# Performance work log

Measured on AMD Instinct MI355X. Metric: run time of the kernel, lower is better.

The kernel has to match this reference:

```python
import jax, jax.numpy as jnp
import numpy as np
from jax import lax


def squash(x, axis=-1):
    sq = jnp.sum(x * x, axis=axis, keepdims=True)
    n = jnp.sqrt(sq)
    return jnp.tanh(n) * x / (n + 1e-8)


def setup_inputs() -> dict:
    key = jax.random.key(0)
    ks = jax.random.split(key, 12)
    B = 2048
    x = jax.random.normal(ks[0], (B, 64, 22, 22), dtype=jnp.float32)
    conv1_w = 0.02 * jax.random.normal(ks[1], (256, 64, 9, 9), dtype=jnp.float32)
    conv1_b = jnp.zeros((256,), jnp.float32)
    pc_w = 0.02 * jax.random.normal(ks[2], (48, 256, 8, 8), dtype=jnp.float32)  # out_channels*num_conv_units=8*6
    pc_b = jnp.zeros((48,), jnp.float32)
    W_digit = 0.01 * jax.random.normal(ks[3], (1, 2, 96, 16, 8), dtype=jnp.float32)  # (1,out_caps,in_caps,out_dim,in_dim)
    dec_w1 = 0.05 * jax.random.normal(ks[4], (512, 32), dtype=jnp.float32)  # in = out_dim*num_classes = 16*2
    dec_b1 = jnp.zeros((512,), jnp.float32)
    dec_w2 = 0.03 * jax.random.normal(ks[5], (1024, 512), dtype=jnp.float32)
    dec_b2 = jnp.zeros((1024,), jnp.float32)
    dec_w3 = 0.03 * jax.random.normal(ks[6], (256, 1024), dtype=jnp.float32)  # fusion_dim=256
    dec_b3 = jnp.zeros((256,), jnp.float32)
    return dict(x=x, conv1_w=conv1_w, conv1_b=conv1_b, pc_w=pc_w, pc_b=pc_b,
                W_digit=W_digit, dec_w1=dec_w1, dec_b1=dec_b1, dec_w2=dec_w2,
                dec_b2=dec_b2, dec_w3=dec_w3, dec_b3=dec_b3)


def reference(x, conv1_w, conv1_b, pc_w, pc_b, W_digit,
              dec_w1, dec_b1, dec_w2, dec_b2, dec_w3, dec_b3):
    DN = ('NCHW', 'OIHW', 'NCHW')
    NUM_ROUTING = 2
    OUT_CAPS = 2
    # conv1 + relu: (B,64,22,22) -> (B,256,14,14)
    out = lax.conv_general_dilated(x, conv1_w, (1, 1), 'VALID', dimension_numbers=DN)
    out = jax.nn.relu(out + conv1_b[None, :, None, None])
    # primary caps conv: -> (B,48,4,4)
    pc = lax.conv_general_dilated(out, pc_w, (2, 2), 'VALID', dimension_numbers=DN)
    pc = pc + pc_b[None, :, None, None]
    B = pc.shape[0]
    u = squash(pc.reshape(B, -1, 8), axis=-1)  # (B, 96, 8)
    # u_hat: W (out_caps,in_caps,out_dim,in_dim) x u (B,in_caps,in_dim) -> (B,out_caps,in_caps,out_dim)
    u_hat = jnp.einsum('oidk,bik->boid', W_digit[0], u)
    tmp = lax.stop_gradient(u_hat)
    b = jnp.zeros((B, OUT_CAPS, 96, 1), u_hat.dtype)
    for _ in range(NUM_ROUTING - 1):
        c = jax.nn.softmax(b, axis=1)                     # over out_caps
        v = squash(jnp.sum(c * tmp, axis=2))              # (B,out_caps,out_dim)
        b = jnp.einsum('boid,bod->boi', tmp, v)[..., None]
    c = jax.nn.softmax(b, axis=1)
    v = squash(jnp.sum(c * u_hat, axis=2))                # (B,out_caps,out_dim)
    logits = jnp.linalg.norm(v, axis=-1)                  # (B,out_caps)
    pred = jax.nn.one_hot(jnp.argmax(logits, axis=1), OUT_CAPS, dtype=v.dtype)  # (B,out_caps)
    h = (v * pred[:, :, None]).reshape(B, -1)             # (B, out_caps*out_dim)
    h = jax.nn.relu(h @ dec_w1.T + dec_b1)
    h = jax.nn.relu(h @ dec_w2.T + dec_b2)
    recon = jax.nn.sigmoid(h @ dec_w3.T + dec_b3)
    return logits, recon
```

## Files before the change

### kernel.cpp

```cpp
#include <hip/hip_runtime.h>
#include <cstdint>
#include <cstddef>

typedef short short8 __attribute__((ext_vector_type(8)));
typedef short short4v __attribute__((ext_vector_type(4)));
typedef float f32x16 __attribute__((ext_vector_type(16)));
typedef float f32x4 __attribute__((ext_vector_type(4)));

__device__ inline unsigned short bf16_rne(float x) {
    unsigned u = __float_as_uint(x);
    unsigned r = u + 0x7FFFu + ((u >> 16) & 1u);
    return (unsigned short)(r >> 16);
}
__device__ inline float bf16_to_f(unsigned short h) {
    return __uint_as_float(((unsigned)h) << 16);
}

__global__ void reorder_wf_kernel(const float* __restrict__ w, unsigned short* __restrict__ wf) {
    int idx = blockIdx.x * 256 + threadIdx.x;
    if (idx >= 324 * 8 * 64 * 8) return;
    int j   = idx & 7;
    int l   = (idx >> 3) & 63;
    int nc  = (idx >> 9) & 7;
    int ksg = idx >> 12;
    int cc  = ksg / 81;
    int tap = ksg - cc * 81;
    int ci  = cc * 16 + ((l >> 5) << 3) + j;
    int co  = nc * 32 + (l & 31);
    float v = w[(co * 64 + ci) * 81 + tap];
    unsigned short hi = bf16_rne(v);
    unsigned short lo = bf16_rne(v - bf16_to_f(hi));
    size_t base = ((size_t)(ksg * 8 + nc)) * 1024;
    wf[base + l * 8 + j]       = hi;
    wf[base + 512 + l * 8 + j] = lo;
}

__global__ void reorder_pcwf_kernel(const float* __restrict__ w, unsigned short* __restrict__ wf) {
    int idx = blockIdx.x * 256 + threadIdx.x;
    if (idx >= 1572864) return;
    int j     = idx & 7;
    int l     = (idx >> 3) & 63;
    int plane = (idx >> 9) & 1;
    int rest  = idx >> 10;
    int ct    = rest % 3;
    int rest2 = rest / 3;
    int tap   = rest2 & 63;
    int cc    = rest2 >> 6;
    int co = ct * 16 + (l & 15);
    int ci = cc * 32 + ((l >> 4) << 3) + j;
    float v = w[((size_t)co * 256 + ci) * 64 + tap];
    unsigned short hi = bf16_rne(v);
    unsigned short out = plane ? bf16_rne(v - bf16_to_f(hi)) : hi;
    wf[idx] = out;
}

#define RS 36

__global__ __launch_bounds__(256, 2) void conv1_mfma_kernel(
    const float* __restrict__ x, const unsigned short* __restrict__ wf,
    const float* __restrict__ b1, float* __restrict__ c1o, int c0)
{
    __shared__ unsigned short Xs[484 * RS];
    const int t  = threadIdx.x;
    const int l  = t & 63;
    const int w  = t >> 6;
    const int il = blockIdx.x >> 1;
    const int nb = blockIdx.x & 1;
    const int bg = c0 + il;
    const int ncol = nb * 4 + w;
    const int lane31 = l & 31;
    const int kg = l >> 5;
    const int co = ncol * 32 + lane31;
    const float bias = b1[co];

    int am[7];
#pragma unroll
    for (int mt = 0; mt < 7; ++mt) {
        int p  = mt * 32 + lane31;
        int pp = (p < 196) ? p : 0;
        int oh = pp / 14, ow = pp - oh * 14;
        am[mt] = (oh * 22 + ow) * RS + kg * 8;
    }
    const char* wfb = (const char*)wf;
    const int boff = ncol * 2048 + l * 16;

    f32x16 acc[7];
#pragma unroll
    for (int mt = 0; mt < 7; ++mt) acc[mt] = (f32x16)(0.f);

    for (int cc = 0; cc < 4; ++cc) {
        __syncthreads();
        for (int i = t; i < 16 * 121; i += 256) {
            int ci = i / 121;
            int sq = i - ci * 121;
            const float4 v = *(const float4*)(x + ((size_t)bg * 64 + cc * 16 + ci) * 484 + sq * 4);
#pragma unroll
            for (int e = 0; e < 4; ++e) {
                float xv = ((const float*)&v)[e];
                unsigned short hi = bf16_rne(xv);
                unsigned short lo = bf16_rne(xv - bf16_to_f(hi));
                int s = sq * 4 + e;
                Xs[s * RS + ci]      = hi;
                Xs[s * RS + 16 + ci] = lo;
            }
        }
        __syncthreads();

        const int ksgb = cc * 81;
        short8 bh0 = *(const short8*)(wfb + (size_t)ksgb * 16384 + boff);
        short8 bl0 = *(const short8*)(wfb + (size_t)ksgb * 16384 + 1024 + boff);

        for (int tap = 0; tap < 81; ++tap) {
            int kn = ksgb + tap + 1; if (kn > 323) kn = 323;
            short8 bh1 = *(const short8*)(wfb + (size_t)kn * 16384 + boff);
            short8 bl1 = *(const short8*)(wfb + (size_t)kn * 16384 + 1024 + boff);

            const int kh = tap / 9, kw = tap - kh * 9;
            const int toff = (kh * 22 + kw) * RS;
#pragma unroll
            for (int mt = 0; mt < 7; ++mt) {
                const int a = am[mt] + toff;
                short4v h0 = *(const short4v*)(Xs + a);
                short4v h1 = *(const short4v*)(Xs + a + 4);
                short4v q0 = *(const short4v*)(Xs + a + 16);
                short4v q1 = *(const short4v*)(Xs + a + 20);
                short8 Ah = __builtin_shufflevector(h0, h1, 0, 1, 2, 3, 4, 5, 6, 7);
                short8 Al = __builtin_shufflevector(q0, q1, 0, 1, 2, 3, 4, 5, 6, 7);
                acc[mt] = __builtin_amdgcn_mfma_f32_32x32x16_bf16(Ah, bh0, acc[mt], 0, 0, 0);
                acc[mt] = __builtin_amdgcn_mfma_f32_32x32x16_bf16(Ah, bl0, acc[mt], 0, 0, 0);
                acc[mt] = __builtin_amdgcn_mfma_f32_32x32x16_bf16(Al, bh0, acc[mt], 0, 0, 0);
                acc[mt] = __builtin_amdgcn_mfma_f32_32x32x16_bf16(Al, bl0, acc[mt], 0, 0, 0);
            }
            bh0 = bh1; bl0 = bl1;
        }
    }

#pragma unroll
    for (int mt = 0; mt < 7; ++mt) {
#pragma unroll
        for (int r = 0; r < 16; ++r) {
            int p = mt * 32 + (r & 3) + ((r >> 2) << 3) + kg * 4;
            if (p < 196) {
                float v = acc[mt][r] + bias;
                c1o[((size_t)il * 196 + p) * 256 + co] = fmaxf(v, 0.f);
            }
        }
    }
}

#define PC_RS 36

__global__ __launch_bounds__(256, 2) void pc_mfma_kernel(
    const float* __restrict__ c1o, const unsigned short* __restrict__ pcwf,
    const float* __restrict__ pcb, float* __restrict__ pco)
{
    __shared__ unsigned short Xh[196 * PC_RS];
    __shared__ unsigned short Xl[196 * PC_RS];
    const int t  = threadIdx.x;
    const int l  = t & 63;
    const int w  = t >> 6;
    const int il = blockIdx.x;
    const int pos = l & 15;
    const int kg  = l >> 4;
    const int oh = pos >> 2, ow = pos & 3;
    const char* wb = (const char*)pcwf;

    f32x4 acc0 = (f32x4)(0.f), acc1 = (f32x4)(0.f), acc2 = (f32x4)(0.f);

    for (int cc = 0; cc < 8; ++cc) {
        __syncthreads();
        for (int q = t; q < 1568; q += 256) {
            int p  = q >> 3;
            int c4 = (q & 7) << 2;
            const float4 v = *(const float4*)(c1o + ((size_t)il * 196 + p) * 256 + cc * 32 + c4);
            short4v hv, lv;
#pragma unroll
            for (int e = 0; e < 4; ++e) {
                float xv = ((const float*)&v)[e];
                unsigned short hi = bf16_rne(xv);
                hv[e] = (short)hi;
                lv[e] = (short)bf16_rne(xv - bf16_to_f(hi));
            }
            *(short4v*)(Xh + p * PC_RS + c4) = hv;
            *(short4v*)(Xl + p * PC_RS + c4) = lv;
        }
        __syncthreads();

        short8 Bh0[3], Bl0[3], Bh1[3], Bl1[3];
        {
            const char* bp = wb + ((size_t)(cc * 64 + w) * 6) * 1024 + l * 16;
#pragma unroll
            for (int ct = 0; ct < 3; ++ct) {
                Bh0[ct] = *(const short8*)(bp + ct * 2048);
                Bl0[ct] = *(const short8*)(bp + ct * 2048 + 1024);
            }
        }
        for (int tt = 0; tt < 16; ++tt) {
            const int tap = tt * 4 + w;
            const int tapn = (tt == 15) ? tap : (tap + 4);
            const char* bpn = wb + ((size_t)(cc * 64 + tapn) * 6) * 1024 + l * 16;
#pragma unroll
            for (int ct = 0; ct < 3; ++ct) {
                Bh1[ct] = *(const short8*)(bpn + ct * 2048);
                Bl1[ct] = *(const short8*)(bpn + ct * 2048 + 1024);
            }
            const int kh = tap >> 3, kw = tap & 7;
            const int pix = (2 * oh + kh) * 14 + (2 * ow + kw);
            const int a = pix * PC_RS + kg * 8;
            short4v h0 = *(const short4v*)(Xh + a);
            short4v h1 = *(const short4v*)(Xh + a + 4);
            short4v q0 = *(const short4v*)(Xl + a);
            short4v q1 = *(const short4v*)(Xl + a + 4);
            short8 Ah = __builtin_shufflevector(h0, h1, 0, 1, 2, 3, 4, 5, 6, 7);
            short8 Al = __builtin_shufflevector(q0, q1, 0, 1, 2, 3, 4, 5, 6, 7);

            acc0 = __builtin_amdgcn_mfma_f32_16x16x32_bf16(Ah, Bh0[0], acc0, 0, 0, 0);
            acc0 = __builtin_amdgcn_mfma_f32_16x16x32_bf16(Ah, Bl0[0], acc0, 0, 0, 0);
            acc0 = __builtin_amdgcn_mfma_f32_16x16x32_bf16(Al, Bh0[0], acc0, 0, 0, 0);
            acc0 = __builtin_amdgcn_mfma_f32_16x16x32_bf16(Al, Bl0[0], acc0, 0, 0, 0);
            acc1 = __builtin_amdgcn_mfma_f32_16x16x32_bf16(Ah, Bh0[1], acc1, 0, 0, 0);
            acc1 = __builtin_amdgcn_mfma_f32_16x16x32_bf16(Ah, Bl0[1], acc1, 0, 0, 0);
            acc1 = __builtin_amdgcn_mfma_f32_16x16x32_bf16(Al, Bh0[1], acc1, 0, 0, 0);
            acc1 = __builtin_amdgcn_mfma_f32_16x16x32_bf16(Al, Bl0[1], acc1, 0, 0, 0);
            acc2 = __builtin_amdgcn_mfma_f32_16x16x32_bf16(Ah, Bh0[2], acc2, 0, 0, 0);
            acc2 = __builtin_amdgcn_mfma_f32_16x16x32_bf16(Ah, Bl0[2], acc2, 0, 0, 0);
            acc2 = __builtin_amdgcn_mfma_f32_16x16x32_bf16(Al, Bh0[2], acc2, 0, 0, 0);
            acc2 = __builtin_amdgcn_mfma_f32_16x16x32_bf16(Al, Bl0[2], acc2, 0, 0, 0);
#pragma unroll
            for (int ct = 0; ct < 3; ++ct) { Bh0[ct] = Bh1[ct]; Bl0[ct] = Bl1[ct]; }
        }
    }

    __syncthreads();
    float* R = (float*)Xh;
#pragma unroll
    for (int ct = 0; ct < 3; ++ct) {
        f32x4 a = (ct == 0) ? acc0 : (ct == 1) ? acc1 : acc2;
#pragma unroll
        for (int r = 0; r < 4; ++r)
            R[(((w * 3 + ct) * 64) + l) * 4 + r] = a[r];
    }
    __syncthreads();
    for (int idx = t; idx < 768; idx += 256) {
        int pp = idx & 15, co = idx >> 4;
        int ct = co >> 4, col = co & 15;
        int lane = ((pp >> 2) << 4) | col, reg = pp & 3;
        float s = 0.f;
#pragma unroll
        for (int w4 = 0; w4 < 4; ++w4)
            s += R[(((w4 * 3 + ct) * 64) + lane) * 4 + reg];
        pco[(size_t)il * 768 + idx] = s + pcb[co];
    }
}

__global__ __launch_bounds__(64) void caps_kernel(
    const float* __restrict__ pco, const float* __restrict__ Wd,
    float* __restrict__ logits_out, float* __restrict__ hbuf, int c0) {
    __shared__ float u_s[96][8];
    __shared__ float uh[2][96][16];
    __shared__ float vv[2][16];
    __shared__ float cc2[2][96];
    __shared__ float lg_s[2];
    const int t = threadIdx.x;
    const int il = blockIdx.x;

    for (int cap = t; cap < 96; cap += 64) {
        float xr[8];
        float n2 = 0.f;
#pragma unroll
        for (int k = 0; k < 8; ++k) {
            xr[k] = pco[(size_t)il * 768 + cap * 8 + k];
            n2 = fmaf(xr[k], xr[k], n2);
        }
        float nr = sqrtf(n2);
        float sc = tanhf(nr) / (nr + 1e-8f);
#pragma unroll
        for (int k = 0; k < 8; ++k) u_s[cap][k] = xr[k] * sc;
    }
    __syncthreads();
    for (int j = t; j < 3072; j += 64) {
        int d = j & 15;
        int oi = j >> 4;
        int i = oi % 96;
        int o = oi / 96;
        float acc = 0.f;
#pragma unroll
        for (int k = 0; k < 8; ++k)
            acc = fmaf(Wd[(size_t)j * 8 + k], u_s[i][k], acc);
        uh[o][i][d] = acc;
    }
    __syncthreads();
    const int o = t >> 4, d = t & 15;
    if (t < 32) {
        float s = 0.f;
        for (int i = 0; i < 96; ++i) s += 0.5f * uh[o][i][d];
        float n2 = s * s;
        n2 += __shfl_xor(n2, 1); n2 += __shfl_xor(n2, 2);
        n2 += __shfl_xor(n2, 4); n2 += __shfl_xor(n2, 8);
        float nr = sqrtf(n2);
        vv[o][d] = tanhf(nr) * s / (nr + 1e-8f);
    }
    __syncthreads();
    for (int j = t; j < 192; j += 64) {
        int oo = j / 96, ii = j - oo * 96;
        float bsum = 0.f;
#pragma unroll
        for (int dd = 0; dd < 16; ++dd)
            bsum = fmaf(uh[oo][ii][dd], vv[oo][dd], bsum);
        cc2[oo][ii] = bsum;
    }
    __syncthreads();
    for (int ii = t; ii < 96; ii += 64) {
        float b0 = cc2[0][ii], b1v = cc2[1][ii];
        float m = fmaxf(b0, b1v);
        float e0 = expf(b0 - m), e1 = expf(b1v - m);
        float inv = 1.f / (e0 + e1);
        cc2[0][ii] = e0 * inv;
        cc2[1][ii] = e1 * inv;
    }
    __syncthreads();
    if (t < 32) {
        float s = 0.f;
        for (int i = 0; i < 96; ++i) s = fmaf(cc2[o][i], uh[o][i][d], s);
        float n2 = s * s;
        n2 += __shfl_xor(n2, 1); n2 += __shfl_xor(n2, 2);
        n2 += __shfl_xor(n2, 4); n2 += __shfl_xor(n2, 8);
        float nr = sqrtf(n2);
        float v = tanhf(nr) * s / (nr + 1e-8f);
        float n2v = v * v;
        n2v += __shfl_xor(n2v, 1); n2v += __shfl_xor(n2v, 2);
        n2v += __shfl_xor(n2v, 4); n2v += __shfl_xor(n2v, 8);
        vv[o][d] = v;
        if (d == 0) {
            float lg = sqrtf(n2v);
            lg_s[o] = lg;
            logits_out[(size_t)(c0 + il) * 2 + o] = lg;
        }
    }
    __syncthreads();
    if (t < 32) {
        int ostar = (lg_s[1] > lg_s[0]) ? 1 : 0;
        hbuf[(size_t)il * 32 + t] = (o == ostar) ? vv[o][d] : 0.f;
    }
}

__global__ __launch_bounds__(256) void fc_kernel(
    const float* __restrict__ in, const float* __restrict__ W,
    const float* __restrict__ bias, float* __restrict__ out,
    int M, int N, int K, int act) {
    __shared__ float As[64][33];
    __shared__ float Bs[64][33];
    const int t = threadIdx.x;
    const int m0 = blockIdx.x * 64, n0 = blockIdx.y * 64;
    const int tn = t & 15, tm = t >> 4;
    float acc[4][4];
#pragma unroll
    for (int i = 0; i < 4; ++i)
#pragma unroll
        for (int j = 0; j < 4; ++j) acc[i][j] = 0.f;
    const int rr = t >> 2, c8 = (t & 3) * 8;
    for (int kc = 0; kc < K; kc += 32) {
        __syncthreads();
        const int mrow = m0 + rr;
#pragma unroll
        for (int q = 0; q < 8; ++q) {
            As[rr][c8 + q] = (mrow < M) ? in[(size_t)mrow * K + kc + c8 + q] : 0.f;
            Bs[rr][c8 + q] = W[(size_t)(n0 + rr) * K + kc + c8 + q];
        }
        __syncthreads();
#pragma unroll
        for (int k = 0; k < 32; ++k) {
            float av[4], bv[4];
#pragma unroll
            for (int i = 0; i < 4; ++i) av[i] = As[tm * 4 + i][k];
#pragma unroll
            for (int j = 0; j < 4; ++j) bv[j] = Bs[tn * 4 + j][k];
#pragma unroll
            for (int i = 0; i < 4; ++i)
#pragma unroll
                for (int j = 0; j < 4; ++j) acc[i][j] = fmaf(av[i], bv[j], acc[i][j]);
        }
    }
#pragma unroll
    for (int i = 0; i < 4; ++i) {
        int m = m0 + tm * 4 + i;
        if (m < M) {
#pragma unroll
            for (int j = 0; j < 4; ++j) {
                int nn = n0 + tn * 4 + j;
                float v = acc[i][j] + bias[nn];
                if (act == 0) v = fmaxf(v, 0.f);
                else v = 1.f / (1.f + expf(-v));
                out[(size_t)m * N + nn] = v;
            }
        }
    }
}

extern "C" void kernel_launch(void* const* d_in, const int* in_sizes, int n_in,
                              void* d_out, int out_size, void* d_ws, size_t ws_size,
                              hipStream_t stream) {
    const float* x    = (const float*)d_in[0];
    const float* w1   = (const float*)d_in[1];
    const float* b1   = (const float*)d_in[2];
    const float* pcw  = (const float*)d_in[3];
    const float* pcb  = (const float*)d_in[4];
    const float* Wd   = (const float*)d_in[5];
    const float* dw1  = (const float*)d_in[6];
    const float* db1  = (const float*)d_in[7];
    const float* dw2  = (const float*)d_in[8];
    const float* db2  = (const float*)d_in[9];
    const float* dw3  = (const float*)d_in[10];
    const float* db3  = (const float*)d_in[11];
    float* out = (float*)d_out;

    const int B = 2048;
    float* ws = (float*)d_ws;
    unsigned short* wf = (unsigned short*)ws;
    unsigned short* pcwf = (unsigned short*)(ws + 1327104);
    float* dyn  = ws + 1327104 + 786432;

    const long long base_floats = 1327104LL + 786432LL;
    const long long per_img = 50176 + 768 + 32 + 512 + 1024;
    long long avail = (long long)(ws_size / 4) - base_floats;
    int CH;
    if (avail < per_img) CH = 1;
    else CH = (int)(avail / per_img);
    if (CH > B) CH = B;

    reorder_wf_kernel<<<(324 * 8 * 64 * 8 + 255) / 256, 256, 0, stream>>>(w1, wf);
    reorder_pcwf_kernel<<<(1572864 + 255) / 256, 256, 0, stream>>>(pcw, pcwf);

    float* c1o  = dyn;
    float* pco  = c1o  + (size_t)CH * 50176;
    float* hbuf = pco  + (size_t)CH * 768;
    float* h1   = hbuf + (size_t)CH * 32;
    float* h2   = h1   + (size_t)CH * 512;

    for (int c0 = 0; c0 < B; c0 += CH) {
        int n = B - c0; if (n > CH) n = CH;
        conv1_mfma_kernel<<<n * 2, 256, 0, stream>>>(x, wf, b1, c1o, c0);
        pc_mfma_kernel<<<n, 256, 0, stream>>>(c1o, pcwf, pcb, pco);
        caps_kernel<<<n, 64, 0, stream>>>(pco, Wd, out, hbuf, c0);
        fc_kernel<<<dim3((n + 63) / 64, 8),  256, 0, stream>>>(hbuf, dw1, db1, h1, n, 512, 32, 0);
        fc_kernel<<<dim3((n + 63) / 64, 16), 256, 0, stream>>>(h1,   dw2, db2, h2, n, 1024, 512, 0);
        fc_kernel<<<dim3((n + 63) / 64, 4),  256, 0, stream>>>(h2,   dw3, db3, out + 4096 + (size_t)c0 * 256, n, 256, 1024, 1);
    }
}
```

Before: 3.823 ms.

## Merge conv1 column halves into one 512-thread block with prefetched input staging

Conv1 now runs one 512-thread block per image covering all 256 output channels, so each image's input is converted to split-bf16 and staged in shared memory once instead of twice. The next 16-channel input chunk is loaded into registers while the MFMA loop runs on the current chunk, then converted and stored after a barrier. Row stride padding goes from 36 to 40 so A fragments can be read as single 16-byte LDS loads. The cost is higher register pressure from the prefetch buffer, one block per CU at launch bounds 512, and a different bank-conflict pattern from the new stride.

Result: no change. 3.807 ms (-0.4%).

```diff
diff --git a/kernel.cpp b/kernel.cpp
--- a/kernel.cpp
+++ b/kernel.cpp
@@ -54,23 +54,21 @@
     wf[idx] = out;
 }
 
-#define RS 36
-
-__global__ __launch_bounds__(256, 2) void conv1_mfma_kernel(
+#define RS 40
+
+__global__ __launch_bounds__(512, 1) void conv1_mfma_kernel(
     const float* __restrict__ x, const unsigned short* __restrict__ wf,
     const float* __restrict__ b1, float* __restrict__ c1o, int c0)
 {
-    __shared__ unsigned short Xs[484 * RS];
+    __shared__ __align__(16) unsigned short Xs[484 * RS];
     const int t  = threadIdx.x;
     const int l  = t & 63;
     const int w  = t >> 6;
-    const int il = blockIdx.x >> 1;
-    const int nb = blockIdx.x & 1;
+    const int il = blockIdx.x;
     const int bg = c0 + il;
-    const int ncol = nb * 4 + w;
     const int lane31 = l & 31;
     const int kg = l >> 5;
-    const int co = ncol * 32 + lane31;
+    const int co = w * 32 + lane31;
     const float bias = b1[co];
 
     int am[7];
@@ -82,29 +80,46 @@
         am[mt] = (oh * 22 + ow) * RS + kg * 8;
     }
     const char* wfb = (const char*)wf;
-    const int boff = ncol * 2048 + l * 16;
+    const int boff = w * 2048 + l * 16;
+
+    const int sidx = t >> 2;
+    const int sblk = t & 3;
 
     f32x16 acc[7];
 #pragma unroll
     for (int mt = 0; mt < 7; ++mt) acc[mt] = (f32x16)(0.f);
 
+#pragma unroll
+    for (int r = 0; r < 4; ++r) {
+        int s = sidx + r * 128;
+        if (s < 484) {
+            short4v hv, lv;
+#pragma unroll
+            for (int e = 0; e < 4; ++e) {
+                float xv = x[((size_t)bg * 64 + sblk * 4 + e) * 484 + s];
+                unsigned short hi = bf16_rne(xv);
+                hv[e] = (short)hi;
+                lv[e] = (short)bf16_rne(xv - bf16_to_f(hi));
+            }
+            *(short4v*)(Xs + s * RS + sblk * 4)      = hv;
+            *(short4v*)(Xs + s * RS + 16 + sblk * 4) = lv;
+        }
+    }
+    __syncthreads();
+
     for (int cc = 0; cc < 4; ++cc) {
-        __syncthreads();
-        for (int i = t; i < 16 * 121; i += 256) {
-            int ci = i / 121;
-            int sq = i - ci * 121;
-            const float4 v = *(const float4*)(x + ((size_t)bg * 64 + cc * 16 + ci) * 484 + sq * 4);
-#pragma unroll
-            for (int e = 0; e < 4; ++e) {
-                float xv = ((const float*)&v)[e];
-                unsigned short hi = bf16_rne(xv);
-                unsigned short lo = bf16_rne(xv - bf16_to_f(hi));
-                int s = sq * 4 + e;
-                Xs[s * RS + ci]      = hi;
-                Xs[s * RS + 16 + ci] = lo;
-            }
-        }
-        __syncthreads();
+        float vx[4][4];
+        if (cc < 3) {
+#pragma unroll
+            for (int r = 0; r < 4; ++r) {
+                int s = sidx + r * 128;
+                if (s < 484) {
+#pragma unroll
+                    for (int e = 0; e < 4; ++e)
+                        vx[r][e] = x[((size_t)bg * 64 + (cc + 1) * 16 + sblk * 4 + e) * 484 + s];
+                }
+            }
+        }
 
         const int ksgb = cc * 81;
         short8 bh0 = *(const short8*)(wfb + (size_t)ksgb * 16384 + boff);
@@ -120,18 +135,35 @@
 #pragma unroll
             for (int mt = 0; mt < 7; ++mt) {
                 const int a = am[mt] + toff;
-                short4v h0 = *(const short4v*)(Xs + a);
-                short4v h1 = *(const short4v*)(Xs + a + 4);
-                short4v q0 = *(const short4v*)(Xs + a + 16);
-                short4v q1 = *(const short4v*)(Xs + a + 20);
-                short8 Ah = __builtin_shufflevector(h0, h1, 0, 1, 2, 3, 4, 5, 6, 7);
-                short8 Al = __builtin_shufflevector(q0, q1, 0, 1, 2, 3, 4, 5, 6, 7);
+                short8 Ah = *(const short8*)(Xs + a);
+                short8 Al = *(const short8*)(Xs + a + 16);
                 acc[mt] = __builtin_amdgcn_mfma_f32_32x32x16_bf16(Ah, bh0, acc[mt], 0, 0, 0);
                 acc[mt] = __builtin_amdgcn_mfma_f32_32x32x16_bf16(Ah, bl0, acc[mt], 0, 0, 0);
                 acc[mt] = __builtin_amdgcn_mfma_f32_32x32x16_bf16(Al, bh0, acc[mt], 0, 0, 0);
                 acc[mt] = __builtin_amdgcn_mfma_f32_32x32x16_bf16(Al, bl0, acc[mt], 0, 0, 0);
             }
             bh0 = bh1; bl0 = bl1;
+        }
+
+        if (cc < 3) {
+            __syncthreads();
+#pragma unroll
+            for (int r = 0; r < 4; ++r) {
+                int s = sidx + r * 128;
+                if (s < 484) {
+                    short4v hv, lv;
+#pragma unroll
+                    for (int e = 0; e < 4; ++e) {
+                        float xv = vx[r][e];
+                        unsigned short hi = bf16_rne(xv);
+                        hv[e] = (short)hi;
+                        lv[e] = (short)bf16_rne(xv - bf16_to_f(hi));
+                    }
+                    *(short4v*)(Xs + s * RS + sblk * 4)      = hv;
+                    *(short4v*)(Xs + s * RS + 16 + sblk * 4) = lv;
+                }
+            }
+            __syncthreads();
         }
     }
 
@@ -439,7 +471,7 @@
 
     for (int c0 = 0; c0 < B; c0 += CH) {
         int n = B - c0; if (n > CH) n = CH;
-        conv1_mfma_kernel<<<n * 2, 256, 0, stream>>>(x, wf, b1, c1o, c0);
+        conv1_mfma_kernel<<<n, 512, 0, stream>>>(x, wf, b1, c1o, c0);
         pc_mfma_kernel<<<n, 256, 0, stream>>>(c1o, pcwf, pcb, pco);
         caps_kernel<<<n, 64, 0, stream>>>(pco, Wd, out, hbuf, c0);
         fc_kernel<<<dim3((n + 63) / 64, 8),  256, 0, stream>>>(hbuf, dw1, db1, h1, n, 512, 32, 0);
```

## Split conv1 M-tiles across 512-thread blocks and vectorize LDS staging

Applied to the files above, without the earlier changes.

Conv1 blocks now use 512 threads, and each wave handles 4 or 3 of the 7 M-tiles instead of all 7. This halves the accumulator registers per wave and raises occupancy and latency hiding. The LDS row stride grows to 40 so A fragments can be read with one 16-byte load. Staging now writes short4 vectors per spatial position instead of scalar shorts, which trades coalesced float4 global reads for strided scalar loads. Each weight fragment is now fetched by twice as many waves, adding global/L2 traffic for B operands.

Measured after the change: 4.089 ms. 1.07x slower.

```diff
diff --git a/kernel.cpp b/kernel.cpp
--- a/kernel.cpp
+++ b/kernel.cpp
@@ -54,98 +54,111 @@
     wf[idx] = out;
 }
 
-#define RS 36
-
-__global__ __launch_bounds__(256, 2) void conv1_mfma_kernel(
-    const float* __restrict__ x, const unsigned short* __restrict__ wf,
-    const float* __restrict__ b1, float* __restrict__ c1o, int c0)
+#define RS 40
+
+template<int MTC>
+__device__ __forceinline__ void conv1_body(
+    unsigned short* Xs, const float* __restrict__ x,
+    const unsigned short* __restrict__ wf, const float* __restrict__ b1,
+    float* __restrict__ c1o, int bg, int il, int t, int mtbase, int ncol)
 {
-    __shared__ unsigned short Xs[484 * RS];
-    const int t  = threadIdx.x;
-    const int l  = t & 63;
-    const int w  = t >> 6;
-    const int il = blockIdx.x >> 1;
-    const int nb = blockIdx.x & 1;
-    const int bg = c0 + il;
-    const int ncol = nb * 4 + w;
+    const int l = t & 63;
     const int lane31 = l & 31;
     const int kg = l >> 5;
     const int co = ncol * 32 + lane31;
     const float bias = b1[co];
 
-    int am[7];
-#pragma unroll
-    for (int mt = 0; mt < 7; ++mt) {
-        int p  = mt * 32 + lane31;
+    int am[MTC];
+#pragma unroll
+    for (int i = 0; i < MTC; ++i) {
+        int p = (mtbase + i) * 32 + lane31;
         int pp = (p < 196) ? p : 0;
         int oh = pp / 14, ow = pp - oh * 14;
-        am[mt] = (oh * 22 + ow) * RS + kg * 8;
+        am[i] = (oh * 22 + ow) * RS + kg * 8;
     }
     const char* wfb = (const char*)wf;
     const int boff = ncol * 2048 + l * 16;
 
-    f32x16 acc[7];
-#pragma unroll
-    for (int mt = 0; mt < 7; ++mt) acc[mt] = (f32x16)(0.f);
+    const int sidx = t >> 2;
+    const int sblk = t & 3;
+
+    f32x16 acc[MTC];
+#pragma unroll
+    for (int i = 0; i < MTC; ++i) acc[i] = (f32x16)(0.f);
 
     for (int cc = 0; cc < 4; ++cc) {
+        if (cc > 0) __syncthreads();
+#pragma unroll
+        for (int r = 0; r < 4; ++r) {
+            int s = sidx + r * 128;
+            if (s < 484) {
+                short4v hv, lv;
+#pragma unroll
+                for (int e = 0; e < 4; ++e) {
+                    float xv = x[((size_t)bg * 64 + cc * 16 + sblk * 4 + e) * 484 + s];
+                    unsigned short hi = bf16_rne(xv);
+                    hv[e] = (short)hi;
+                    lv[e] = (short)bf16_rne(xv - bf16_to_f(hi));
+                }
+                *(short4v*)(Xs + s * RS + sblk * 4)      = hv;
+                *(short4v*)(Xs + s * RS + 16 + sblk * 4) = lv;
+            }
+        }
         __syncthreads();
-        for (int i = t; i < 16 * 121; i += 256) {
-            int ci = i / 121;
-            int sq = i - ci * 121;
-            const float4 v = *(const float4*)(x + ((size_t)bg * 64 + cc * 16 + ci) * 484 + sq * 4);
-#pragma unroll
-            for (int e = 0; e < 4; ++e) {
-                float xv = ((const float*)&v)[e];
-                unsigned short hi = bf16_rne(xv);
-                unsigned short lo = bf16_rne(xv - bf16_to_f(hi));
-                int s = sq * 4 + e;
-                Xs[s * RS + ci]      = hi;
-                Xs[s * RS + 16 + ci] = lo;
-            }
-        }
-        __syncthreads();
 
         const int ksgb = cc * 81;
-        short8 bh0 = *(const short8*)(wfb + (size_t)ksgb * 16384 + boff);
-        short8 bl0 = *(const short8*)(wfb + (size_t)ksgb * 16384 + 1024 + boff);
+        const char* bp0 = wfb + (size_t)ksgb * 16384;
+        short8 bh0 = *(const short8*)(bp0 + boff);
+        short8 bl0 = *(const short8*)(bp0 + 1024 + boff);
 
         for (int tap = 0; tap < 81; ++tap) {
             int kn = ksgb + tap + 1; if (kn > 323) kn = 323;
-            short8 bh1 = *(const short8*)(wfb + (size_t)kn * 16384 + boff);
-            short8 bl1 = *(const short8*)(wfb + (size_t)kn * 16384 + 1024 + boff);
+            const char* bpn = wfb + (size_t)kn * 16384;
+            short8 bh1 = *(const short8*)(bpn + boff);
+            short8 bl1 = *(const short8*)(bpn + 1024 + boff);
 
             const int kh = tap / 9, kw = tap - kh * 9;
             const int toff = (kh * 22 + kw) * RS;
 #pragma unroll
-            for (int mt = 0; mt < 7; ++mt) {
-                const int a = am[mt] + toff;
-                short4v h0 = *(const short4v*)(Xs + a);
-                short4v h1 = *(const short4v*)(Xs + a + 4);
-                short4v q0 = *(const short4v*)(Xs + a + 16);
-                short4v q1 = *(const short4v*)(Xs + a + 20);
-                short8 Ah = __builtin_shufflevector(h0, h1, 0, 1, 2, 3, 4, 5, 6, 7);
-                short8 Al = __builtin_shufflevector(q0, q1, 0, 1, 2, 3, 4, 5, 6, 7);
-                acc[mt] = __builtin_amdgcn_mfma_f32_32x32x16_bf16(Ah, bh0, acc[mt], 0, 0, 0);
-                acc[mt] = __builtin_amdgcn_mfma_f32_32x32x16_bf16(Ah, bl0, acc[mt], 0, 0, 0);
-                acc[mt] = __builtin_amdgcn_mfma_f32_32x32x16_bf16(Al, bh0, acc[mt], 0, 0, 0);
-                acc[mt] = __builtin_amdgcn_mfma_f32_32x32x16_bf16(Al, bl0, acc[mt], 0, 0, 0);
+            for (int i = 0; i < MTC; ++i) {
+                const int a = am[i] + toff;
+                short8 Ah = *(const short8*)(Xs + a);
+                short8 Al = *(const short8*)(Xs + a + 16);
+                acc[i] = __builtin_amdgcn_mfma_f32_32x32x16_bf16(Ah, bh0, acc[i], 0, 0, 0);
+                acc[i] = __builtin_amdgcn_mfma_f32_32x32x16_bf16(Ah, bl0, acc[i], 0, 0, 0);
+                acc[i] = __builtin_amdgcn_mfma_f32_32x32x16_bf16(Al, bh0, acc[i], 0, 0, 0);
+                acc[i] = __builtin_amdgcn_mfma_f32_32x32x16_bf16(Al, bl0, acc[i], 0, 0, 0);
             }
             bh0 = bh1; bl0 = bl1;
         }
     }
 
 #pragma unroll
-    for (int mt = 0; mt < 7; ++mt) {
+    for (int i = 0; i < MTC; ++i) {
 #pragma unroll
         for (int r = 0; r < 16; ++r) {
-            int p = mt * 32 + (r & 3) + ((r >> 2) << 3) + kg * 4;
+            int p = (mtbase + i) * 32 + (r & 3) + ((r >> 2) << 3) + kg * 4;
             if (p < 196) {
-                float v = acc[mt][r] + bias;
+                float v = acc[i][r] + bias;
                 c1o[((size_t)il * 196 + p) * 256 + co] = fmaxf(v, 0.f);
             }
         }
     }
+}
+
+__global__ __launch_bounds__(512, 4) void conv1_mfma_kernel(
+    const float* __restrict__ x, const unsigned short* __restrict__ wf,
+    const float* __restrict__ b1, float* __restrict__ c1o, int c0)
+{
+    __shared__ __align__(16) unsigned short Xs[484 * RS];
+    const int t  = threadIdx.x;
+    const int il = blockIdx.x >> 1;
+    const int nb = blockIdx.x & 1;
+    const int bg = c0 + il;
+    const int w  = t >> 6;
+    const int ncol = nb * 4 + (w & 3);
+    if (w < 4) conv1_body<4>(Xs, x, wf, b1, c1o, bg, il, t, 0, ncol);
+    else       conv1_body<3>(Xs, x, wf, b1, c1o, bg, il, t, 4, ncol);
 }
 
 #define PC_RS 36
@@ -439,7 +452,7 @@
 
     for (int c0 = 0; c0 < B; c0 += CH) {
         int n = B - c0; if (n > CH) n = CH;
-        conv1_mfma_kernel<<<n * 2, 256, 0, stream>>>(x, wf, b1, c1o, c0);
+        conv1_mfma_kernel<<<n * 2, 512, 0, stream>>>(x, wf, b1, c1o, c0);
         pc_mfma_kernel<<<n, 256, 0, stream>>>(c1o, pcwf, pcb, pco);
         caps_kernel<<<n, 64, 0, stream>>>(pco, Wd, out, hbuf, c0);
         fc_kernel<<<dim3((n + 63) / 64, 8),  256, 0, stream>>>(hbuf, dw1, db1, h1, n, 512, 32, 0);
```
